# Kernel tuning notes

Hardware: AMD Instinct MI355X
Metric: run time of the kernel (lower is better)

The kernel has to match this reference:

```python
import jax, jax.numpy as jnp
import numpy as np

B, T, D_IN = 1024, 512, 32   # batch, sequence_length, input_dim
H = 512                      # hidden_dim
P = 96                       # prediction_length
D_OUT = 1                    # output_dim


def setup_inputs() -> dict:
    key = jax.random.key(0)
    ks = jax.random.split(key, 24)
    s = 1.0 / np.sqrt(H)  # PyTorch GRU default init scale
    u = lambda k, shape: jax.random.uniform(k, shape, jnp.float32, -s, s)
    inp = {"x": jax.random.normal(ks[0], (B, T, D_IN), jnp.float32)}
    # Encoder GRU: layer0 input D_IN, layer1 input H. Gate order: r, z, n.
    inp["enc_Wih0"] = u(ks[1], (3 * H, D_IN)); inp["enc_Whh0"] = u(ks[2], (3 * H, H))
    inp["enc_bih0"] = u(ks[3], (3 * H,));      inp["enc_bhh0"] = u(ks[4], (3 * H,))
    inp["enc_Wih1"] = u(ks[5], (3 * H, H));    inp["enc_Whh1"] = u(ks[6], (3 * H, H))
    inp["enc_bih1"] = u(ks[7], (3 * H,));      inp["enc_bhh1"] = u(ks[8], (3 * H,))
    # Decoder GRU: layer0 input D_OUT, layer1 input H.
    inp["dec_Wih0"] = u(ks[9], (3 * H, D_OUT)); inp["dec_Whh0"] = u(ks[10], (3 * H, H))
    inp["dec_bih0"] = u(ks[11], (3 * H,));      inp["dec_bhh0"] = u(ks[12], (3 * H,))
    inp["dec_Wih1"] = u(ks[13], (3 * H, H));    inp["dec_Whh1"] = u(ks[14], (3 * H, H))
    inp["dec_bih1"] = u(ks[15], (3 * H,));      inp["dec_bhh1"] = u(ks[16], (3 * H,))
    # Output projection + learned decoder start token.
    inp["out_W"] = u(ks[17], (D_OUT, H)); inp["out_b"] = u(ks[18], (D_OUT,))
    inp["dec_start"] = jnp.zeros((1, 1, D_OUT), jnp.float32)
    return inp


def gru_cell(x, h, Wih, Whh, bih, bhh):
    # PyTorch GRU cell: r,z,n gate order.
    gi = x @ Wih.T + bih          # [B, 3H]
    gh = h @ Whh.T + bhh          # [B, 3H]
    ir, iz, inn = jnp.split(gi, 3, axis=-1)
    hr, hz, hn = jnp.split(gh, 3, axis=-1)
    r = jax.nn.sigmoid(ir + hr)
    z = jax.nn.sigmoid(iz + hz)
    n = jnp.tanh(inn + r * hn)
    return (1.0 - z) * n + z * h


def reference(x,
              enc_Wih0, enc_Whh0, enc_bih0, enc_bhh0,
              enc_Wih1, enc_Whh1, enc_bih1, enc_bhh1,
              dec_Wih0, dec_Whh0, dec_bih0, dec_bhh0,
              dec_Wih1, dec_Whh1, dec_bih1, dec_bhh1,
              out_W, out_b, dec_start):
    Bsz = x.shape[0]
    h0 = jnp.zeros((Bsz, H), x.dtype)

    def enc_step(carry, xt):
        h1, h2 = carry
        h1 = gru_cell(xt, h1, enc_Wih0, enc_Whh0, enc_bih0, enc_bhh0)
        h2 = gru_cell(h1, h2, enc_Wih1, enc_Whh1, enc_bih1, enc_bhh1)
        return (h1, h2), None

    (h1, h2), _ = jax.lax.scan(enc_step, (h0, h0), jnp.swapaxes(x, 0, 1))

    y0 = jnp.broadcast_to(dec_start[0], (Bsz, D_OUT)).astype(x.dtype)

    def dec_step(carry, _):
        d1, d2, y = carry
        d1 = gru_cell(y, d1, dec_Wih0, dec_Whh0, dec_bih0, dec_bhh0)
        d2 = gru_cell(d1, d2, dec_Wih1, dec_Whh1, dec_bih1, dec_bhh1)
        y = d2 @ out_W.T + out_b  # [B, D_OUT]
        return (d1, d2, y), y

    _, ys = jax.lax.scan(dec_step, (h1, h2, y0), None, length=P)
    return jnp.swapaxes(ys, 0, 1)  # [B, P, D_OUT]
```

## Files before the change

kernel.cpp:

```cpp
#include <hip/hip_runtime.h>

#define HD 512
#define BB 1024
#define TT 512
#define PP 96
#define DIN 32
#define KC_H 16
#define NBLK 256
#define GRPB 16

typedef unsigned short u16;
typedef __attribute__((ext_vector_type(8))) short bf16x8;
typedef __attribute__((ext_vector_type(4))) float f32x4;
typedef __attribute__((address_space(3))) unsigned int lds_u32;
typedef __attribute__((address_space(3))) u16 lds_u16;
typedef __attribute__((address_space(1))) unsigned int glb_u32;

#define WAIT_VM(N) asm volatile("s_waitcnt vmcnt(" #N ")" ::: "memory")
__device__ __forceinline__ void bar_raw() { asm volatile("s_barrier" ::: "memory"); }

__device__ __forceinline__ float bf2f(u16 s) {
  return __uint_as_float(((unsigned)s) << 16);
}
__device__ __forceinline__ u16 f2bf_rne(float f) {
  unsigned u = __float_as_uint(f);
  u += 0x7FFF + ((u >> 16) & 1);
  return (u16)(u >> 16);
}
__device__ __forceinline__ float sigm(float v) { return 1.f / (1.f + __expf(-v)); }
__device__ __forceinline__ float tanh_(float a) {
  return 1.f - 2.f / (__expf(2.f * a) + 1.f);
}

__device__ __forceinline__ bf16x8 load_sc16(const u16* p) {
  bf16x8 r;
  asm volatile("global_load_dwordx4 %0, %1, off sc0 sc1" : "=&v"(r) : "v"(p) : "memory");
  return r;
}
__device__ __forceinline__ void store_sc_u16(u16* p, unsigned v) {
  asm volatile("global_store_short %0, %1, off sc0 sc1" :: "v"(p), "v"(v) : "memory");
}
__device__ __forceinline__ void store_sc_f32(float* p, float v) {
  asm volatile("global_store_dword %0, %1, off sc0 sc1" :: "v"(p), "v"(v) : "memory");
}
__device__ __forceinline__ float load_sc_f32w(const float* p) {
  float v;
  asm volatile("global_load_dword %0, %1, off sc0 sc1\ns_waitcnt vmcnt(0)"
               : "=&v"(v) : "v"(p) : "memory");
  return v;
}
__device__ __forceinline__ unsigned load_sc_u32w(const unsigned* p) {
  unsigned v;
  asm volatile("global_load_dword %0, %1, off sc0 sc1\ns_waitcnt vmcnt(0)"
               : "=&v"(v) : "v"(p) : "memory");
  return v;
}
__device__ __forceinline__ void store_h_sc(u16* H, u16* L, size_t idx, float hv) {
  u16 hi = (u16)(__float_as_uint(hv) >> 16);
  u16 lo = f2bf_rne(hv - bf2f(hi));
  store_sc_u16(H + idx, (unsigned)hi);
  store_sc_u16(L + idx, (unsigned)lo);
}

__global__ void pack_w_kernel(const float* __restrict__ W, int K,
                              u16* __restrict__ out) {
  int tid = blockIdx.x * 256 + threadIdx.x;
  int KC = K >> 5;
  int total = 16 * KC * 2 * 6 * 64;
  if (tid >= total) return;
  int lane = tid & 63;
  int rest = tid >> 6;
  int gs = rest % 6; rest /= 6;
  int fc = rest & 1; rest >>= 1;
  int kc = rest % KC;
  int jb = rest / KC;
  int g = gs >> 1, s = gs & 1;
  int j = jb * 32 + fc * 16 + (lane & 15);
  int k = kc * 32 + (lane >> 4) * 8;
  const float* src = W + (size_t)(g * HD + j) * K + k;
  bf16x8 v;
#pragma unroll
  for (int i = 0; i < 8; ++i) {
    float f = src[i];
    u16 hi = f2bf_rne(f);
    v[i] = (short)((s == 0) ? hi : f2bf_rne(f - bf2f(hi)));
  }
  *(bf16x8*)(out + (size_t)tid * 8) = v;
}

struct AF { bf16x8 h; bf16x8 l; };

__device__ __forceinline__ void fence_af(AF& a) {
  asm volatile("" : "+v"(a.h), "+v"(a.l));
}
__device__ __forceinline__ void load_af_sc(AF& a, const u16* aH0, const u16* aL0, int kc) {
  a.h = load_sc16(aH0 + kc * 32);
  a.l = load_sc16(aL0 + kc * 32);
}

__device__ __forceinline__ void mfma_kc_l(const lds_u16* base, int lane, const AF& a,
                                          f32x4& aR, f32x4& aZ, f32x4& aN) {
  typedef __attribute__((address_space(3))) const bf16x8 lds_bf16x8;
  const lds_u16* p = base + lane * 8;
#pragma unroll
  for (int g = 0; g < 3; ++g) {
    f32x4* acc = (g == 0) ? &aR : (g == 1) ? &aZ : &aN;
    bf16x8 whi = *(lds_bf16x8*)(p + (g * 2 + 0) * 512);
    bf16x8 wlo = *(lds_bf16x8*)(p + (g * 2 + 1) * 512);
    *acc = __builtin_amdgcn_mfma_f32_16x16x32_bf16(a.h, whi, *acc, 0, 0, 0);
    *acc = __builtin_amdgcn_mfma_f32_16x16x32_bf16(a.l, whi, *acc, 0, 0, 0);
    *acc = __builtin_amdgcn_mfma_f32_16x16x32_bf16(a.h, wlo, *acc, 0, 0, 0);
  }
}
__device__ __forceinline__ void mfma_kc_g(const u16* base, int lane, const AF& a,
                                          f32x4& aR, f32x4& aZ, f32x4& aN) {
  const u16* p = base + lane * 8;
#pragma unroll
  for (int g = 0; g < 3; ++g) {
    f32x4* acc = (g == 0) ? &aR : (g == 1) ? &aZ : &aN;
    bf16x8 whi = *(const bf16x8*)(p + (g * 2 + 0) * 512);
    bf16x8 wlo = *(const bf16x8*)(p + (g * 2 + 1) * 512);
    *acc = __builtin_amdgcn_mfma_f32_16x16x32_bf16(a.h, whi, *acc, 0, 0, 0);
    *acc = __builtin_amdgcn_mfma_f32_16x16x32_bf16(a.l, whi, *acc, 0, 0, 0);
    *acc = __builtin_amdgcn_mfma_f32_16x16x32_bf16(a.h, wlo, *acc, 0, 0, 0);
  }
}

__device__ __forceinline__ void stage6(const u16* src, u16* dst, int lane) {
#pragma unroll
  for (int j = 0; j < 6; ++j)
    __builtin_amdgcn_global_load_lds((const glb_u32*)(src + j * 512 + lane * 8),
                                     (lds_u32*)(dst + j * 512), 16, 0, 0);
}

template <bool DUAL>
__device__ __forceinline__ void pipe_phase(
    u16* ringb, const u16* Ahi, const u16* Alo,
    const u16* WA, const u16* WB, int row0w, int lane, bool stg, int sfc,
    f32x4* aR, f32x4* aZ, f32x4* aN,
    f32x4* bR, f32x4* bZ, f32x4* bN) {
  const int quad = lane >> 4, n16 = lane & 15;
  const u16* aH0 = Ahi + (size_t)(row0w + n16) * HD + quad * 8;
  const u16* aL0 = Alo + (size_t)(row0w + n16) * HD + quad * 8;
  u16* pb[4] = {ringb, ringb + 12288, ringb + 2 * 12288, ringb + 3 * 12288};
  AF a0, a1, a2, a3;

  auto issueB = [&](int ikc, u16* slot, AF& dst) {
    if (stg) {
      stage6(WA + (size_t)ikc * 6144, slot + sfc * 6144, lane);
      if constexpr (DUAL) stage6(WB + (size_t)ikc * 6144, slot + sfc * 6144 + 3072, lane);
    }
    load_af_sc(dst, aH0, aL0, ikc);
  };
  auto cons = [&](u16* slot, AF& a) {
    fence_af(a);
#pragma unroll
    for (int f = 0; f < 2; ++f) {
      mfma_kc_l((const lds_u16*)(slot + f * 6144), lane, a, aR[f], aZ[f], aN[f]);
      if constexpr (DUAL)
        mfma_kc_l((const lds_u16*)(slot + f * 6144 + 3072), lane, a, bR[f], bZ[f], bN[f]);
    }
  };
  auto wsteady = [&]() {
    if (stg) { if constexpr (DUAL) WAIT_VM(28); else WAIT_VM(16); }
    else WAIT_VM(4);
  };
  auto wtail1 = [&]() {
    if (stg) { if constexpr (DUAL) WAIT_VM(14); else WAIT_VM(8); }
    else WAIT_VM(2);
  };

  WAIT_VM(0);
  issueB(0, pb[0], a0);
  issueB(1, pb[1], a1);
  issueB(2, pb[2], a2);
#pragma unroll 1
  for (int kc = 0; kc < 12; kc += 4) {
    wsteady(); bar_raw(); issueB(kc + 3, pb[3], a3); cons(pb[0], a0);
    wsteady(); bar_raw(); issueB(kc + 4, pb[0], a0); cons(pb[1], a1);
    wsteady(); bar_raw(); issueB(kc + 5, pb[1], a1); cons(pb[2], a2);
    wsteady(); bar_raw(); issueB(kc + 6, pb[2], a2); cons(pb[3], a3);
  }
  wsteady(); bar_raw(); issueB(15, pb[3], a3); cons(pb[0], a0);
  wsteady(); bar_raw(); cons(pb[1], a1);
  wtail1();  bar_raw(); cons(pb[2], a2);
  WAIT_VM(0); bar_raw(); cons(pb[3], a3);
}

__device__ __forceinline__ void x_phase(const float* x, int t, const u16* Wp,
                                        int jb, int row0w, int lane,
                                        f32x4* aR, f32x4* aZ, f32x4* aN) {
  const int quad = lane >> 4, n16 = lane & 15;
  AF ax;
  const float* xp = x + (size_t)(row0w + n16) * (TT * DIN) +
                    (size_t)t * DIN + quad * 8;
  f32x4 v0 = *(const f32x4*)xp;
  f32x4 v1 = *(const f32x4*)(xp + 4);
  bf16x8 hi, lo;
#pragma unroll
  for (int i = 0; i < 8; ++i) {
    float f = (i < 4) ? v0[i] : v1[i - 4];
    u16 h = (u16)(__float_as_uint(f) >> 16);
    hi[i] = (short)h;
    lo[i] = (short)f2bf_rne(f - bf2f(h));
  }
  ax.h = hi;
  ax.l = lo;
#pragma unroll
  for (int f = 0; f < 2; ++f)
    mfma_kc_g(Wp + ((size_t)jb * 2 + f) * 3072, lane, ax, aR[f], aZ[f], aN[f]);
}

__device__ __forceinline__ void gbar(unsigned* gen, unsigned target) {
  WAIT_VM(0);
  __syncthreads();
  if (threadIdx.x == 0) {
    atomicAdd(gen, 1u);
    while (load_sc_u32w(gen) < target) __builtin_amdgcn_s_sleep(2);
  }
  __syncthreads();
}

__device__ __forceinline__ void gru_epi_reg(
    const float* bi, const float* bh, float (*ht)[4],
    u16* hnH, u16* hnL, int col0, int row0w, int quad,
    const f32x4* aR, const f32x4* aZ, const f32x4* aNX, const f32x4* aNH) {
#pragma unroll
  for (int f = 0; f < 2; ++f) {
    const int col = col0 + f * 16;
    const float bir = bi[col],          bhr = bh[col];
    const float biz = bi[HD + col],     bhz = bh[HD + col];
    const float bin = bi[2 * HD + col], bhn = bh[2 * HD + col];
#pragma unroll
    for (int r = 0; r < 4; ++r) {
      const int row = row0w + quad * 4 + r;
      const size_t idx = (size_t)row * HD + col;
      float rr = sigm(aR[f][r] + bir + bhr);
      float zz = sigm(aZ[f][r] + biz + bhz);
      float nn = tanh_(aNX[f][r] + bin + rr * (aNH[f][r] + bhn));
      float hv = (1.f - zz) * nn + zz * ht[f][r];
      ht[f][r] = hv;
      store_h_sc(hnH, hnL, idx, hv);
    }
  }
}

__global__ __launch_bounds__(256, 1)
void gru_persistent_kernel(
    const float* x,
    const u16* pkX0, const u16* pkH0, const float* bi0, const float* bh0,
    const u16* pkX1, const u16* pkH1, const float* bi1, const float* bh1,
    const u16* pkD0H, const float* dbi0, const float* dbh0, const float* dW0,
    const u16* pkD1I, const u16* pkD1H, const float* dbi1, const float* dbh1,
    const float* outW, const float* outb, const float* dstart,
    u16* h1aH, u16* h1aL, u16* h1bH, u16* h1bL,
    u16* h2aH, u16* h2aL, u16* h2bH, u16* h2bL,
    float* yfull, float* dout, unsigned* gen) {
  __shared__ u16 ring[4][12288];
  const int b = blockIdx.x;
  const int jb = (b & 7) * 2 + ((b >> 3) & 1);
  const int row0 = (b >> 4) * 64;
  const int tid = threadIdx.x, wave = tid >> 6, lane = tid & 63;
  const int quad = lane >> 4, n16 = lane & 15;
  const bool stg = (wave < 2);
  const int sfc = wave & 1;
  const int row0w = row0 + wave * 16;
  const int col0 = jb * 32 + n16;
  u16* ringb = &ring[0][0];
  const f32x4 z4 = {0.f, 0.f, 0.f, 0.f};
  const size_t woffw = ((size_t)jb * KC_H * 2 + sfc) * 3072;
  unsigned* geng = gen + ((b >> 4) << 6);

  u16 *h1cH = h1aH, *h1cL = h1aL, *h1nH = h1bH, *h1nL = h1bL;
  u16 *h2cH = h2aH, *h2cL = h2aL, *h2nH = h2bH, *h2nL = h2bL;
  float ht1[2][4] = {{0, 0, 0, 0}, {0, 0, 0, 0}};
  float ht2[2][4] = {{0, 0, 0, 0}, {0, 0, 0, 0}};
  unsigned it = 0;

  for (int k = 0; k <= TT; ++k) {
    f32x4 R0[2] = {z4, z4}, Z0[2] = {z4, z4}, NX0[2] = {z4, z4}, NH0[2] = {z4, z4};
    f32x4 R1[2] = {z4, z4}, Z1[2] = {z4, z4}, NX1[2] = {z4, z4}, NH1[2] = {z4, z4};
    if (k > 0 && k < TT) {
      pipe_phase<true>(ringb, h1cH, h1cL, pkH0 + woffw, pkX1 + woffw,
                       row0w, lane, stg, sfc, R0, Z0, NH0, R1, Z1, NX1);
    } else if (k == 0) {
      pipe_phase<false>(ringb, h1cH, h1cL, pkH0 + woffw, pkH0 + woffw,
                        row0w, lane, stg, sfc, R0, Z0, NH0, R1, Z1, NX1);
    } else {
      pipe_phase<false>(ringb, h1cH, h1cL, pkX1 + woffw, pkX1 + woffw,
                        row0w, lane, stg, sfc, R1, Z1, NX1, R0, Z0, NH0);
    }
    if (k < TT) {
      x_phase(x, k, pkX0, jb, row0w, lane, R0, Z0, NX0);
      gru_epi_reg(bi0, bh0, ht1, h1nH, h1nL, col0, row0w, quad, R0, Z0, NX0, NH0);
    }
    if (k > 0) {
      pipe_phase<false>(ringb, h2cH, h2cL, pkH1 + woffw, pkH1 + woffw,
                        row0w, lane, stg, sfc, R1, Z1, NH1, R0, Z0, NX0);
      gru_epi_reg(bi1, bh1, ht2, h2nH, h2nL, col0, row0w, quad, R1, Z1, NX1, NH1);
    }
    gbar(geng, GRPB * (++it));
    if (k < TT) { u16* t0 = h1cH; h1cH = h1nH; h1nH = t0;
                  u16* t1 = h1cL; h1cL = h1nL; h1nL = t1; }
    if (k > 0)  { u16* t0 = h2cH; h2cH = h2nH; h2nH = t0;
                  u16* t1 = h2cL; h2cL = h2nL; h2nL = t1; }
  }

  for (int t = 0; t < PP; ++t) {
    {
      f32x4 R[2] = {z4, z4}, Z[2] = {z4, z4}, NH[2] = {z4, z4};
      f32x4 D0[2] = {z4, z4}, D1[2] = {z4, z4}, D2[2] = {z4, z4};
      pipe_phase<false>(ringb, h1cH, h1cL, pkD0H + woffw, pkD0H + woffw,
                        row0w, lane, stg, sfc, R, Z, NH, D0, D1, D2);
      float yl[4] = {0, 0, 0, 0};
      if (t > 0) {
        const float* yb = yfull + ((t - 1) & 1) * BB;
#pragma unroll
        for (int r = 0; r < 4; ++r) {
          const float* p = yb + (row0w + quad * 4 + r);
          asm volatile("global_load_dword %0, %1, off sc0 sc1"
                       : "=&v"(yl[r]) : "v"(p) : "memory");
        }
        WAIT_VM(0);
#pragma unroll
        for (int r = 0; r < 4; ++r)
          asm volatile("" : "+v"(yl[r]));
      }
      const float ds0 = dstart[0], ob0 = outb[0];
#pragma unroll
      for (int f = 0; f < 2; ++f) {
        const int col = col0 + f * 16;
        const float bir = dbi0[col],          bhr = dbh0[col];
        const float biz = dbi0[HD + col],     bhz = dbh0[HD + col];
        const float bin = dbi0[2 * HD + col], bhn = dbh0[2 * HD + col];
        const float w0r = dW0[col], w0z = dW0[HD + col], w0n = dW0[2 * HD + col];
#pragma unroll
        for (int r = 0; r < 4; ++r) {
          const int row = row0w + quad * 4 + r;
          const size_t idx = (size_t)row * HD + col;
          float yv = (t == 0) ? ds0 : (ob0 + yl[r]);
          if (f == 0 && t > 0 && jb == 0 && n16 == 0)
            dout[(size_t)row * PP + (t - 1)] = yv;
          float rr = sigm(R[f][r] + bir + bhr + yv * w0r);
          float zz = sigm(Z[f][r] + biz + bhz + yv * w0z);
          float nn = tanh_(bin + yv * w0n + rr * (NH[f][r] + bhn));
          float hv = (1.f - zz) * nn + zz * ht1[f][r];
          ht1[f][r] = hv;
          store_h_sc(h1nH, h1nL, idx, hv);
        }
      }
    }
    gbar(geng, GRPB * (++it));
    {
      f32x4 R[2] = {z4, z4}, Z[2] = {z4, z4}, NX[2] = {z4, z4}, NH[2] = {z4, z4};
      f32x4 D0[2] = {z4, z4}, D1[2] = {z4, z4}, D2[2] = {z4, z4};
      pipe_phase<false>(ringb, h1nH, h1nL, pkD1I + woffw, pkD1I + woffw,
                        row0w, lane, stg, sfc, R, Z, NX, D0, D1, D2);
      pipe_phase<false>(ringb, h2cH, h2cL, pkD1H + woffw, pkD1H + woffw,
                        row0w, lane, stg, sfc, R, Z, NH, D0, D1, D2);
      float vs[4] = {0, 0, 0, 0};
#pragma unroll
      for (int f = 0; f < 2; ++f) {
        const int col = col0 + f * 16;
        const float bir = dbi1[col],          bhr = dbh1[col];
        const float biz = dbi1[HD + col],     bhz = dbh1[HD + col];
        const float bin = dbi1[2 * HD + col], bhn = dbh1[2 * HD + col];
        const float wo = outW[col];
#pragma unroll
        for (int r = 0; r < 4; ++r) {
          const int row = row0w + quad * 4 + r;
          const size_t idx = (size_t)row * HD + col;
          float rr = sigm(R[f][r] + bir + bhr);
          float zz = sigm(Z[f][r] + biz + bhz);
          float nn = tanh_(NX[f][r] + bin + rr * (NH[f][r] + bhn));
          float hv = (1.f - zz) * nn + zz * ht2[f][r];
          ht2[f][r] = hv;
          store_h_sc(h2nH, h2nL, idx, hv);
          float v = hv * wo;
#pragma unroll
          for (int off = 1; off < 16; off <<= 1) v += __shfl_xor(v, off, 16);
          vs[r] += v;
        }
      }
      float* yw = yfull + (t & 1) * BB;
      float* yz = yfull + ((t - 1) & 1) * BB;
#pragma unroll
      for (int r = 0; r < 4; ++r) {
        const int row = row0w + quad * 4 + r;
        if (n16 == 0) {
          atomicAdd(yw + row, vs[r]);
          if (t > 0 && jb == 0) store_sc_f32(yz + row, 0.f);
        }
      }
    }
    gbar(geng, GRPB * (++it));
    { u16* t0 = h1cH; h1cH = h1nH; h1nH = t0;
      u16* t1 = h1cL; h1cL = h1nL; h1nL = t1; }
    { u16* t0 = h2cH; h2cH = h2nH; h2nH = t0;
      u16* t1 = h2cL; h2cL = h2nL; h2nL = t1; }
  }

  if ((b & 15) == 0 && tid < 64) {
    int row = row0 + tid;
    float v = load_sc_f32w(yfull + ((PP - 1) & 1) * BB + row);
    dout[(size_t)row * PP + (PP - 1)] = outb[0] + v;
  }
}

extern "C" void kernel_launch(void* const* d_in, const int* in_sizes, int n_in,
                              void* d_out, int out_size, void* d_ws, size_t ws_size,
                              hipStream_t stream) {
  const float* x      = (const float*)d_in[0];
  const float* eW_ih0 = (const float*)d_in[1];
  const float* eW_hh0 = (const float*)d_in[2];
  const float* eb_ih0 = (const float*)d_in[3];
  const float* eb_hh0 = (const float*)d_in[4];
  const float* eW_ih1 = (const float*)d_in[5];
  const float* eW_hh1 = (const float*)d_in[6];
  const float* eb_ih1 = (const float*)d_in[7];
  const float* eb_hh1 = (const float*)d_in[8];
  const float* dW_ih0 = (const float*)d_in[9];
  const float* dW_hh0 = (const float*)d_in[10];
  const float* db_ih0 = (const float*)d_in[11];
  const float* db_hh0 = (const float*)d_in[12];
  const float* dW_ih1 = (const float*)d_in[13];
  const float* dW_hh1 = (const float*)d_in[14];
  const float* db_ih1 = (const float*)d_in[15];
  const float* db_hh1 = (const float*)d_in[16];
  const float* outW   = (const float*)d_in[17];
  const float* outb   = (const float*)d_in[18];
  const float* dstart = (const float*)d_in[19];
  float* out = (float*)d_out;

  char* w = (char*)d_ws;
  size_t off = 0;
  auto carve = [&](size_t bytes) -> void* {
    void* p = w + off;
    off = (off + bytes + 255) & ~(size_t)255;
    return p;
  };
  u16* h1aH = (u16*)carve((size_t)BB * HD * 2); u16* h1aL = (u16*)carve((size_t)BB * HD * 2);
  u16* h1bH = (u16*)carve((size_t)BB * HD * 2); u16* h1bL = (u16*)carve((size_t)BB * HD * 2);
  u16* h2aH = (u16*)carve((size_t)BB * HD * 2); u16* h2aL = (u16*)carve((size_t)BB * HD * 2);
  u16* h2bH = (u16*)carve((size_t)BB * HD * 2); u16* h2bL = (u16*)carve((size_t)BB * HD * 2);
  float* yfull = (float*)carve((size_t)2 * BB * 4);
  unsigned* gen = (unsigned*)carve(4096);
  auto carve_pack = [&](int K) -> u16* {
    return (u16*)carve((size_t)3 * HD * K * 2 * 2);
  };
  u16* pk_e0ih = carve_pack(DIN);
  u16* pk_e0hh = carve_pack(HD);
  u16* pk_e1ih = carve_pack(HD);
  u16* pk_e1hh = carve_pack(HD);
  u16* pk_d0hh = carve_pack(HD);
  u16* pk_d1ih = carve_pack(HD);
  u16* pk_d1hh = carve_pack(HD);

  hipMemsetAsync(h1aH, 0, (size_t)BB * HD * 2, stream);
  hipMemsetAsync(h1aL, 0, (size_t)BB * HD * 2, stream);
  hipMemsetAsync(h2aH, 0, (size_t)BB * HD * 2, stream);
  hipMemsetAsync(h2aL, 0, (size_t)BB * HD * 2, stream);
  hipMemsetAsync(yfull, 0, (size_t)2 * BB * 4, stream);
  hipMemsetAsync(gen, 0, 4096, stream);

  auto pack = [&](const float* W, int K, u16* dst) {
    int total = 16 * (K >> 5) * 2 * 6 * 64;
    pack_w_kernel<<<(total + 255) / 256, 256, 0, stream>>>(W, K, dst);
  };
  pack(eW_ih0, DIN, pk_e0ih);
  pack(eW_hh0, HD, pk_e0hh);
  pack(eW_ih1, HD, pk_e1ih);
  pack(eW_hh1, HD, pk_e1hh);
  pack(dW_hh0, HD, pk_d0hh);
  pack(dW_ih1, HD, pk_d1ih);
  pack(dW_hh1, HD, pk_d1hh);

  gru_persistent_kernel<<<NBLK, 256, 0, stream>>>(
      x, pk_e0ih, pk_e0hh, eb_ih0, eb_hh0,
      pk_e1ih, pk_e1hh, eb_ih1, eb_hh1,
      pk_d0hh, db_ih0, db_hh0, dW_ih0,
      pk_d1ih, pk_d1hh, db_ih1, db_hh1,
      outW, outb, dstart,
      h1aH, h1aL, h1bH, h1bL, h2aH, h2aL, h2bH, h2bL,
      yfull, out, gen);
}
```

Measured before the change: 16.92 ms.

## Merge GRU matmul phases into one multi-stream pipeline with all-wave staging

Replaces the single or dual weight-stream pipeline with a generic pipeline that stages several weight matrices and several activation operands per k-chunk. Encoder layer-1 recurrent and input matmuls, and layer-0 recurrent, now run in one pass. Decoder layer-1 input and recurrent matmuls are merged the same way. Staging of weights into LDS is spread across all four waves instead of two. The aim is fewer pipeline fill and drain phases and barriers per timestep. In exchange, the three-stream case drops to a depth-3 ring so it fits in LDS, and more vector-memory operations are in flight.

After: 16.27 ms. -3.8%, faster.

```diff
diff --git a/kernel.cpp b/kernel.cpp
--- a/kernel.cpp
+++ b/kernel.cpp
@@ -18,6 +18,15 @@
 
 #define WAIT_VM(N) asm volatile("s_waitcnt vmcnt(" #N ")" ::: "memory")
 __device__ __forceinline__ void bar_raw() { asm volatile("s_barrier" ::: "memory"); }
+
+template <int N> __device__ __forceinline__ void wvm() {
+  if constexpr (N == 0) WAIT_VM(0);
+  else if constexpr (N == 5) WAIT_VM(5);
+  else if constexpr (N == 10) WAIT_VM(10);
+  else if constexpr (N == 13) WAIT_VM(13);
+  else if constexpr (N == 20) WAIT_VM(20);
+  else if constexpr (N == 26) WAIT_VM(26);
+}
 
 __device__ __forceinline__ float bf2f(u16 s) {
   return __uint_as_float(((unsigned)s) << 16);
@@ -88,110 +97,130 @@
   *(bf16x8*)(out + (size_t)tid * 8) = v;
 }
 
-struct AF { bf16x8 h; bf16x8 l; };
-
-__device__ __forceinline__ void fence_af(AF& a) {
-  asm volatile("" : "+v"(a.h), "+v"(a.l));
-}
-__device__ __forceinline__ void load_af_sc(AF& a, const u16* aH0, const u16* aL0, int kc) {
-  a.h = load_sc16(aH0 + kc * 32);
-  a.l = load_sc16(aL0 + kc * 32);
-}
-
-__device__ __forceinline__ void mfma_kc_l(const lds_u16* base, int lane, const AF& a,
-                                          f32x4& aR, f32x4& aZ, f32x4& aN) {
+template <int NA> struct AFN { bf16x8 h[NA]; bf16x8 l[NA]; };
+template <int NA>
+__device__ __forceinline__ void fence_afn(AFN<NA>& a) {
+#pragma unroll
+  for (int n = 0; n < NA; ++n)
+    asm volatile("" : "+v"(a.h[n]), "+v"(a.l[n]));
+}
+
+__device__ __forceinline__ void mfma_kc9(const lds_u16* base, int lane,
+                                         bf16x8 ah, bf16x8 al,
+                                         f32x4& R, f32x4& Z, f32x4& N) {
   typedef __attribute__((address_space(3))) const bf16x8 lds_bf16x8;
   const lds_u16* p = base + lane * 8;
 #pragma unroll
   for (int g = 0; g < 3; ++g) {
-    f32x4* acc = (g == 0) ? &aR : (g == 1) ? &aZ : &aN;
+    f32x4* a = (g == 0) ? &R : (g == 1) ? &Z : &N;
     bf16x8 whi = *(lds_bf16x8*)(p + (g * 2 + 0) * 512);
     bf16x8 wlo = *(lds_bf16x8*)(p + (g * 2 + 1) * 512);
-    *acc = __builtin_amdgcn_mfma_f32_16x16x32_bf16(a.h, whi, *acc, 0, 0, 0);
-    *acc = __builtin_amdgcn_mfma_f32_16x16x32_bf16(a.l, whi, *acc, 0, 0, 0);
-    *acc = __builtin_amdgcn_mfma_f32_16x16x32_bf16(a.h, wlo, *acc, 0, 0, 0);
-  }
-}
-__device__ __forceinline__ void mfma_kc_g(const u16* base, int lane, const AF& a,
-                                          f32x4& aR, f32x4& aZ, f32x4& aN) {
+    *a = __builtin_amdgcn_mfma_f32_16x16x32_bf16(ah, whi, *a, 0, 0, 0);
+    *a = __builtin_amdgcn_mfma_f32_16x16x32_bf16(al, whi, *a, 0, 0, 0);
+    *a = __builtin_amdgcn_mfma_f32_16x16x32_bf16(ah, wlo, *a, 0, 0, 0);
+  }
+}
+__device__ __forceinline__ void mfma_kc9_g(const u16* base, int lane,
+                                           bf16x8 ah, bf16x8 al,
+                                           f32x4& R, f32x4& Z, f32x4& N) {
   const u16* p = base + lane * 8;
 #pragma unroll
   for (int g = 0; g < 3; ++g) {
-    f32x4* acc = (g == 0) ? &aR : (g == 1) ? &aZ : &aN;
+    f32x4* a = (g == 0) ? &R : (g == 1) ? &Z : &N;
     bf16x8 whi = *(const bf16x8*)(p + (g * 2 + 0) * 512);
     bf16x8 wlo = *(const bf16x8*)(p + (g * 2 + 1) * 512);
-    *acc = __builtin_amdgcn_mfma_f32_16x16x32_bf16(a.h, whi, *acc, 0, 0, 0);
-    *acc = __builtin_amdgcn_mfma_f32_16x16x32_bf16(a.l, whi, *acc, 0, 0, 0);
-    *acc = __builtin_amdgcn_mfma_f32_16x16x32_bf16(a.h, wlo, *acc, 0, 0, 0);
-  }
-}
-
-__device__ __forceinline__ void stage6(const u16* src, u16* dst, int lane) {
-#pragma unroll
-  for (int j = 0; j < 6; ++j)
-    __builtin_amdgcn_global_load_lds((const glb_u32*)(src + j * 512 + lane * 8),
-                                     (lds_u32*)(dst + j * 512), 16, 0, 0);
-}
-
-template <bool DUAL>
-__device__ __forceinline__ void pipe_phase(
-    u16* ringb, const u16* Ahi, const u16* Alo,
-    const u16* WA, const u16* WB, int row0w, int lane, bool stg, int sfc,
-    f32x4* aR, f32x4* aZ, f32x4* aN,
-    f32x4* bR, f32x4* bZ, f32x4* bN) {
+    *a = __builtin_amdgcn_mfma_f32_16x16x32_bf16(ah, whi, *a, 0, 0, 0);
+    *a = __builtin_amdgcn_mfma_f32_16x16x32_bf16(al, whi, *a, 0, 0, 0);
+    *a = __builtin_amdgcn_mfma_f32_16x16x32_bf16(ah, wlo, *a, 0, 0, 0);
+  }
+}
+
+template <int NS, int NA, int DEPTH>
+__device__ __forceinline__ void pipeN(
+    u16* ringb,
+    const u16* (&Ahi)[NA], const u16* (&Alo)[NA],
+    const u16* (&Wjb)[NS], const int (&ai)[NS],
+    f32x4* (&acc)[NS][3],
+    int row0w, int lane, int wave) {
+  constexpr int B = NS * 3 + 2 * NA;
+  constexpr int SLOT = NS * 6144;
   const int quad = lane >> 4, n16 = lane & 15;
-  const u16* aH0 = Ahi + (size_t)(row0w + n16) * HD + quad * 8;
-  const u16* aL0 = Alo + (size_t)(row0w + n16) * HD + quad * 8;
-  u16* pb[4] = {ringb, ringb + 12288, ringb + 2 * 12288, ringb + 3 * 12288};
-  AF a0, a1, a2, a3;
-
-  auto issueB = [&](int ikc, u16* slot, AF& dst) {
-    if (stg) {
-      stage6(WA + (size_t)ikc * 6144, slot + sfc * 6144, lane);
-      if constexpr (DUAL) stage6(WB + (size_t)ikc * 6144, slot + sfc * 6144 + 3072, lane);
-    }
-    load_af_sc(dst, aH0, aL0, ikc);
+  const u16* aH[NA]; const u16* aL[NA];
+#pragma unroll
+  for (int n = 0; n < NA; ++n) {
+    aH[n] = Ahi[n] + (size_t)(row0w + n16) * HD + quad * 8;
+    aL[n] = Alo[n] + (size_t)(row0w + n16) * HD + quad * 8;
+  }
+  const u16* srcB[NS * 3]; int dstO[NS * 3];
+#pragma unroll
+  for (int i = 0; i < NS * 3; ++i) {
+    const int p = wave * (NS * 3) + i;
+    const int s = p / 12, r = p % 12, f2 = r / 6, j = r % 6;
+    const int co = f2 * 3072 + j * 512;
+    srcB[i] = Wjb[s] + co + lane * 8;
+    dstO[i] = s * 6144 + co;
+  }
+  u16* pb[DEPTH];
+#pragma unroll
+  for (int d = 0; d < DEPTH; ++d) pb[d] = ringb + d * SLOT;
+  AFN<NA> af[DEPTH];
+
+  auto issueB = [&](int ikc, int si) {
+#pragma unroll
+    for (int i = 0; i < NS * 3; ++i)
+      __builtin_amdgcn_global_load_lds(
+          (const glb_u32*)(srcB[i] + (size_t)ikc * 6144),
+          (lds_u32*)(pb[si] + dstO[i]), 16, 0, 0);
+#pragma unroll
+    for (int n = 0; n < NA; ++n) {
+      af[si].h[n] = load_sc16(aH[n] + ikc * 32);
+      af[si].l[n] = load_sc16(aL[n] + ikc * 32);
+    }
   };
-  auto cons = [&](u16* slot, AF& a) {
-    fence_af(a);
-#pragma unroll
-    for (int f = 0; f < 2; ++f) {
-      mfma_kc_l((const lds_u16*)(slot + f * 6144), lane, a, aR[f], aZ[f], aN[f]);
-      if constexpr (DUAL)
-        mfma_kc_l((const lds_u16*)(slot + f * 6144 + 3072), lane, a, bR[f], bZ[f], bN[f]);
-    }
+  auto cons = [&](int si) {
+    fence_afn(af[si]);
+#pragma unroll
+    for (int s = 0; s < NS; ++s)
+#pragma unroll
+      for (int f = 0; f < 2; ++f)
+        mfma_kc9((const lds_u16*)(pb[si] + s * 6144 + f * 3072), lane,
+                 af[si].h[ai[s]], af[si].l[ai[s]],
+                 acc[s][0][f], acc[s][1][f], acc[s][2][f]);
   };
-  auto wsteady = [&]() {
-    if (stg) { if constexpr (DUAL) WAIT_VM(28); else WAIT_VM(16); }
-    else WAIT_VM(4);
-  };
-  auto wtail1 = [&]() {
-    if (stg) { if constexpr (DUAL) WAIT_VM(14); else WAIT_VM(8); }
-    else WAIT_VM(2);
-  };
 
   WAIT_VM(0);
-  issueB(0, pb[0], a0);
-  issueB(1, pb[1], a1);
-  issueB(2, pb[2], a2);
+#pragma unroll
+  for (int p = 0; p < DEPTH - 1; ++p) issueB(p, p);
+  if constexpr (DEPTH == 4) {
 #pragma unroll 1
-  for (int kc = 0; kc < 12; kc += 4) {
-    wsteady(); bar_raw(); issueB(kc + 3, pb[3], a3); cons(pb[0], a0);
-    wsteady(); bar_raw(); issueB(kc + 4, pb[0], a0); cons(pb[1], a1);
-    wsteady(); bar_raw(); issueB(kc + 5, pb[1], a1); cons(pb[2], a2);
-    wsteady(); bar_raw(); issueB(kc + 6, pb[2], a2); cons(pb[3], a3);
-  }
-  wsteady(); bar_raw(); issueB(15, pb[3], a3); cons(pb[0], a0);
-  wsteady(); bar_raw(); cons(pb[1], a1);
-  wtail1();  bar_raw(); cons(pb[2], a2);
-  WAIT_VM(0); bar_raw(); cons(pb[3], a3);
+    for (int kc = 0; kc < 12; kc += 4) {
+      wvm<2 * B>(); bar_raw(); issueB(kc + 3, 3); cons(0);
+      wvm<2 * B>(); bar_raw(); issueB(kc + 4, 0); cons(1);
+      wvm<2 * B>(); bar_raw(); issueB(kc + 5, 1); cons(2);
+      wvm<2 * B>(); bar_raw(); issueB(kc + 6, 2); cons(3);
+    }
+    wvm<2 * B>(); bar_raw(); issueB(15, 3); cons(0);
+    wvm<2 * B>(); bar_raw(); cons(1);
+    wvm<B>();     bar_raw(); cons(2);
+    wvm<0>();     bar_raw(); cons(3);
+  } else {
+#pragma unroll 1
+    for (int kc = 0; kc < 12; kc += 3) {
+      wvm<B>(); bar_raw(); issueB(kc + 2, 2); cons(0);
+      wvm<B>(); bar_raw(); issueB(kc + 3, 0); cons(1);
+      wvm<B>(); bar_raw(); issueB(kc + 4, 1); cons(2);
+    }
+    wvm<B>(); bar_raw(); issueB(14, 2); cons(0);
+    wvm<B>(); bar_raw(); issueB(15, 0); cons(1);
+    wvm<B>(); bar_raw(); cons(2);
+    wvm<0>(); bar_raw(); cons(0);
+  }
 }
 
 __device__ __forceinline__ void x_phase(const float* x, int t, const u16* Wp,
                                         int jb, int row0w, int lane,
                                         f32x4* aR, f32x4* aZ, f32x4* aN) {
   const int quad = lane >> 4, n16 = lane & 15;
-  AF ax;
   const float* xp = x + (size_t)(row0w + n16) * (TT * DIN) +
                     (size_t)t * DIN + quad * 8;
   f32x4 v0 = *(const f32x4*)xp;
@@ -204,11 +233,10 @@
     hi[i] = (short)h;
     lo[i] = (short)f2bf_rne(f - bf2f(h));
   }
-  ax.h = hi;
-  ax.l = lo;
 #pragma unroll
   for (int f = 0; f < 2; ++f)
-    mfma_kc_g(Wp + ((size_t)jb * 2 + f) * 3072, lane, ax, aR[f], aZ[f], aN[f]);
+    mfma_kc9_g(Wp + ((size_t)jb * 2 + f) * 3072, lane, hi, lo,
+               aR[f], aZ[f], aN[f]);
 }
 
 __device__ __forceinline__ void gbar(unsigned* gen, unsigned target) {
@@ -256,19 +284,23 @@
     u16* h1aH, u16* h1aL, u16* h1bH, u16* h1bL,
     u16* h2aH, u16* h2aL, u16* h2bH, u16* h2bL,
     float* yfull, float* dout, unsigned* gen) {
-  __shared__ u16 ring[4][12288];
+  __shared__ u16 ring[3 * 3 * 6144];
   const int b = blockIdx.x;
   const int jb = (b & 7) * 2 + ((b >> 3) & 1);
   const int row0 = (b >> 4) * 64;
   const int tid = threadIdx.x, wave = tid >> 6, lane = tid & 63;
   const int quad = lane >> 4, n16 = lane & 15;
-  const bool stg = (wave < 2);
-  const int sfc = wave & 1;
   const int row0w = row0 + wave * 16;
   const int col0 = jb * 32 + n16;
-  u16* ringb = &ring[0][0];
+  u16* ringb = &ring[0];
   const f32x4 z4 = {0.f, 0.f, 0.f, 0.f};
-  const size_t woffw = ((size_t)jb * KC_H * 2 + sfc) * 3072;
+  const size_t jbs = (size_t)jb * (KC_H * 2 * 3072);
+  const u16* pkH0j = pkH0 + jbs;
+  const u16* pkX1j = pkX1 + jbs;
+  const u16* pkH1j = pkH1 + jbs;
+  const u16* pkD0Hj = pkD0H + jbs;
+  const u16* pkD1Ij = pkD1I + jbs;
+  const u16* pkD1Hj = pkD1H + jbs;
   unsigned* geng = gen + ((b >> 4) << 6);
 
   u16 *h1cH = h1aH, *h1cL = h1aL, *h1nH = h1bH, *h1nL = h1bL;
@@ -281,22 +313,32 @@
     f32x4 R0[2] = {z4, z4}, Z0[2] = {z4, z4}, NX0[2] = {z4, z4}, NH0[2] = {z4, z4};
     f32x4 R1[2] = {z4, z4}, Z1[2] = {z4, z4}, NX1[2] = {z4, z4}, NH1[2] = {z4, z4};
     if (k > 0 && k < TT) {
-      pipe_phase<true>(ringb, h1cH, h1cL, pkH0 + woffw, pkX1 + woffw,
-                       row0w, lane, stg, sfc, R0, Z0, NH0, R1, Z1, NX1);
+      const u16* Ah[2] = {h1cH, h2cH};
+      const u16* Al[2] = {h1cL, h2cL};
+      const u16* Wv[3] = {pkH0j, pkX1j, pkH1j};
+      const int ai3[3] = {0, 0, 1};
+      f32x4* ac[3][3] = {{R0, Z0, NH0}, {R1, Z1, NX1}, {R1, Z1, NH1}};
+      pipeN<3, 2, 3>(ringb, Ah, Al, Wv, ai3, ac, row0w, lane, wave);
     } else if (k == 0) {
-      pipe_phase<false>(ringb, h1cH, h1cL, pkH0 + woffw, pkH0 + woffw,
-                        row0w, lane, stg, sfc, R0, Z0, NH0, R1, Z1, NX1);
+      const u16* Ah[1] = {h1cH};
+      const u16* Al[1] = {h1cL};
+      const u16* Wv[1] = {pkH0j};
+      const int ai1[1] = {0};
+      f32x4* ac[1][3] = {{R0, Z0, NH0}};
+      pipeN<1, 1, 4>(ringb, Ah, Al, Wv, ai1, ac, row0w, lane, wave);
     } else {
-      pipe_phase<false>(ringb, h1cH, h1cL, pkX1 + woffw, pkX1 + woffw,
-                        row0w, lane, stg, sfc, R1, Z1, NX1, R0, Z0, NH0);
+      const u16* Ah[2] = {h1cH, h2cH};
+      const u16* Al[2] = {h1cL, h2cL};
+      const u16* Wv[2] = {pkX1j, pkH1j};
+      const int ai2[2] = {0, 1};
+      f32x4* ac[2][3] = {{R1, Z1, NX1}, {R1, Z1, NH1}};
+      pipeN<2, 2, 4>(ringb, Ah, Al, Wv, ai2, ac, row0w, lane, wave);
     }
     if (k < TT) {
       x_phase(x, k, pkX0, jb, row0w, lane, R0, Z0, NX0);
       gru_epi_reg(bi0, bh0, ht1, h1nH, h1nL, col0, row0w, quad, R0, Z0, NX0, NH0);
     }
     if (k > 0) {
-      pipe_phase<false>(ringb, h2cH, h2cL, pkH1 + woffw, pkH1 + woffw,
-                        row0w, lane, stg, sfc, R1, Z1, NH1, R0, Z0, NX0);
       gru_epi_reg(bi1, bh1, ht2, h2nH, h2nL, col0, row0w, quad, R1, Z1, NX1, NH1);
     }
     gbar(geng, GRPB * (++it));
@@ -309,9 +351,14 @@
   for (int t = 0; t < PP; ++t) {
     {
       f32x4 R[2] = {z4, z4}, Z[2] = {z4, z4}, NH[2] = {z4, z4};
-      f32x4 D0[2] = {z4, z4}, D1[2] = {z4, z4}, D2[2] = {z4, z4};
-      pipe_phase<false>(ringb, h1cH, h1cL, pkD0H + woffw, pkD0H + woffw,
-                        row0w, lane, stg, sfc, R, Z, NH, D0, D1, D2);
+      {
+        const u16* Ah[1] = {h1cH};
+        const u16* Al[1] = {h1cL};
+        const u16* Wv[1] = {pkD0Hj};
+        const int ai1[1] = {0};
+        f32x4* ac[1][3] = {{R, Z, NH}};
+        pipeN<1, 1, 4>(ringb, Ah, Al, Wv, ai1, ac, row0w, lane, wave);
+      }
       float yl[4] = {0, 0, 0, 0};
       if (t > 0) {
         const float* yb = yfull + ((t - 1) & 1) * BB;
@@ -353,11 +400,14 @@
     gbar(geng, GRPB * (++it));
     {
       f32x4 R[2] = {z4, z4}, Z[2] = {z4, z4}, NX[2] = {z4, z4}, NH[2] = {z4, z4};
-      f32x4 D0[2] = {z4, z4}, D1[2] = {z4, z4}, D2[2] = {z4, z4};
-      pipe_phase<false>(ringb, h1nH, h1nL, pkD1I + woffw, pkD1I + woffw,
-                        row0w, lane, stg, sfc, R, Z, NX, D0, D1, D2);
-      pipe_phase<false>(ringb, h2cH, h2cL, pkD1H + woffw, pkD1H + woffw,
-                        row0w, lane, stg, sfc, R, Z, NH, D0, D1, D2);
+      {
+        const u16* Ah[2] = {h1nH, h2cH};
+        const u16* Al[2] = {h1nL, h2cL};
+        const u16* Wv[2] = {pkD1Ij, pkD1Hj};
+        const int ai2[2] = {0, 1};
+        f32x4* ac[2][3] = {{R, Z, NX}, {R, Z, NH}};
+        pipeN<2, 2, 4>(ringb, Ah, Al, Wv, ai2, ac, row0w, lane, wave);
+      }
       float vs[4] = {0, 0, 0, 0};
 #pragma unroll
       for (int f = 0; f < 2; ++f) {
```
